# Optimization experiments

Measured on AMD Instinct MI355X. Metric: run time of the kernel, lower is better.

## Reference

```python
import jax, jax.numpy as jnp
import numpy as np

N_ROOMS = 128
N = 2 + N_ROOMS          # 2 external wall nodes + room nodes
T = 131072               # number of evaluation times
DT = 30.0                # seconds between evaluations
Q_LIM = 500.0
K_SCALE = 1e-5           # physical scaling of sigmoid(params) -> conductances [1/s]
DAY = 86400.0
TOUT_N = 1100            # hourly outside-temperature table covering the horizon


def setup_inputs() -> dict:
    key = jax.random.key(0)
    k1, k2, k3, k4 = jax.random.split(key, 4)
    t_eval = jnp.arange(T, dtype=jnp.float32) * DT
    params = jax.random.uniform(k1, (N * N,), dtype=jnp.float32)      # torch.rand init
    heating = jax.random.normal(k2, (N_ROOMS, 3), dtype=jnp.float32)  # torch.randn init
    B = jnp.zeros((N, 1 + N_ROOMS), dtype=jnp.float32)
    B = B.at[:, 0].set(jax.random.uniform(k3, (N,), dtype=jnp.float32) * 1e-5)  # Tout coupling
    B = B.at[2:, 1:].set(jnp.eye(N_ROOMS, dtype=jnp.float32) * 1e-6)           # heat input per room
    tout_t = jnp.arange(TOUT_N, dtype=jnp.float32) * 3600.0
    tout_v = 10.0 + 5.0 * jax.random.normal(k4, (TOUT_N,), dtype=jnp.float32)
    return {"t_eval": t_eval, "params": params, "heating": heating, "B": B,
            "tout_t": tout_t, "tout_v": tout_v}


def _forward(t_eval, params, heating, B, tout_t, tout_v):
    # transform + physical scaling of parameters -> RC conductance matrix A
    theta = jax.nn.sigmoid(params) * K_SCALE
    K = theta.reshape(N, N)
    d = jnp.diag(K)
    Koff = K - jnp.diag(d)
    A = Koff - jnp.diag(Koff.sum(axis=1) + d)   # Metzler, nonpositive row sums -> stable

    # transform + heat scaling -> continuous heating profile Qrms_continuous
    Q_avg = jax.nn.sigmoid(heating[:, 0]) * Q_LIM
    phase = heating[:, 1]
    sharp = heating[:, 2]

    t0 = t_eval[0]
    te = t_eval - t0
    two_pi = 2.0 * jnp.pi

    def Tout(t):  # Tout_continuous (linear interp, like scipy interp1d)
        return jnp.interp(t + t0, tout_t, tout_v)

    def Qf(t):    # smooth periodic heating schedule per room
        return Q_avg * jax.nn.sigmoid(sharp * jnp.sin(two_pi * (t + t0) / DAY + phase))

    def f(t, x):  # dx/dt = A @ x + B @ u
        u = jnp.concatenate([Tout(t)[None], Qf(t)])[:, None]   # [1+R, 1]
        return A @ x + B @ u

    iv = (Tout(te[0]) + 4.0) * jnp.ones((N, 1), dtype=jnp.float32)

    def step(x, tt):  # one RK4 step between consecutive evaluation times
        t, dt = tt
        half = dt * 0.5
        k1 = f(t, x)
        k2 = f(t + half, x + half * k1)
        k3 = f(t + half, x + half * k2)
        k4 = f(t + dt, x + dt * k3)
        xn = x + (dt / 6.0) * (k1 + 2.0 * k2 + 2.0 * k3 + k4)
        return xn, xn

    ts = te[:-1]
    dts = te[1:] - te[:-1]
    _, xs = jax.lax.scan(step, iv, (ts, dts))
    sol = jnp.concatenate([iv[None], xs], axis=0)   # [T, N, 1]
    return sol[:, 2:]                               # room temperatures only


def reference(t_eval, params, heating, B, tout_t, tout_v):
    return _forward(t_eval, params, heating, B, tout_t, tout_v)
```

## Files before the change

kernel.cpp:

```cpp
#include <hip/hip_runtime.h>
#include <math.h>

#define NPAD 132
#define TSTEPS 131071
#define LCH 128
#define NCH 1024
#define PERIOD 2880
#define OMEGA 7.2722052166430399e-05f

#define OFF_A    0
#define OFF_A2   17160
#define OFF_A3   34320
#define OFF_M    51480
#define OFF_C1   68640
#define OFF_C2   85800
#define OFF_P1   102960
#define OFF_P2   120120
#define OFF_M2   137280
#define OFF_M4   154440
#define OFF_M64  171600
#define OFF_M128 188760
#define OFF_M2K  205920
#define OFF_C1T  223080
#define OFF_C2T  239464
#define OFF_C1B  255848
#define OFF_C2B  255978
#define OFF_C3B  256108
#define OFF_AMP  256238
#define OFF_CPH  256366
#define OFF_SPH  256494
#define OFF_SH   256622
#define OFF_W    256750
#define OFF_G    257920
#define OFF_S64  391040
#define OFF_XB   524160
#define OFF_XB2  657280
#define OFF_SA   923520
#define OFF_GP   931710
#define OFF_GP2  1306110
#define OFF_GP4  1680510
#define OFF_TT   2054910

typedef float f4 __attribute__((ext_vector_type(4)));

#define MLOAD(Q, S) asm volatile("global_load_dwordx4 %0, %1, off offset:" S \
                                 : "=v"(mr[Q]) : "v"(base))
__device__ __forceinline__ void load_mrow(const float* base, f4* mr) {
    MLOAD(0, "0");    MLOAD(1, "16");   MLOAD(2, "32");   MLOAD(3, "48");
    MLOAD(4, "64");   MLOAD(5, "80");   MLOAD(6, "96");   MLOAD(7, "112");
    MLOAD(8, "128");  MLOAD(9, "144");  MLOAD(10, "160"); MLOAD(11, "176");
    MLOAD(12, "192"); MLOAD(13, "208"); MLOAD(14, "224"); MLOAD(15, "240");
    MLOAD(16, "256"); MLOAD(17, "272"); MLOAD(18, "288"); MLOAD(19, "304");
    MLOAD(20, "320"); MLOAD(21, "336"); MLOAD(22, "352"); MLOAD(23, "368");
    MLOAD(24, "384"); MLOAD(25, "400"); MLOAD(26, "416"); MLOAD(27, "432");
    MLOAD(28, "448"); MLOAD(29, "464"); MLOAD(30, "480"); MLOAD(31, "496");
    MLOAD(32, "512");
    asm volatile("s_waitcnt vmcnt(0)" ::: "memory");
    __builtin_amdgcn_sched_barrier(0);
}

__device__ __forceinline__ float sigm(float x) { return 1.0f / (1.0f + expf(-x)); }

__device__ __forceinline__ float interp_tout(float t, const float* __restrict__ tv) {
    float u = t * (1.0f / 3600.0f);
    int idx = (int)u;
    if (idx > 1098) idx = 1098;
    float fr = u - (float)idx;
    float v0 = tv[idx];
    return v0 + fr * (tv[idx + 1] - v0);
}

__global__ __launch_bounds__(256) void build_A_kernel(
    const float* __restrict__ params, const float* __restrict__ heating,
    const float* __restrict__ Bm, const float* __restrict__ tout_v,
    float* __restrict__ ws, float* __restrict__ out) {
    const int tid = threadIdx.x;
    float* A = ws + OFF_A;

    for (int idx = tid; idx < 130 * 130; idx += 256) {
        int r = idx / 130, c = idx - r * 130;
        A[r * NPAD + c] = sigm(params[idx]) * 1e-5f;
    }
    for (int r = tid; r < 130; r += 256) { A[r * NPAD + 130] = 0.f; A[r * NPAD + 131] = 0.f; }
    __syncthreads();
    for (int r = tid; r < 130; r += 256) {
        float s = 0.0f;
        for (int k = 0; k < 130; ++k) s += A[r * NPAD + k];
        A[r * NPAD + r] = -s;
    }
    for (int i = tid; i < 128; i += 256) {
        float bd = Bm[(2 + i) * 129 + (1 + i)];
        ws[OFF_AMP + i] = sigm(heating[i * 3]) * 500.0f * bd;
        float ph = heating[i * 3 + 1];
        ws[OFF_CPH + i] = cosf(ph);
        ws[OFF_SPH + i] = sinf(ph);
        ws[OFF_SH + i]  = heating[i * 3 + 2];
    }
    float iv = tout_v[0] + 4.0f;
    for (int i = tid; i < 128; i += 256) out[i] = iv;
    for (int r = tid; r < 130; r += 256) ws[OFF_XB + r] = iv;
}

__global__ __launch_bounds__(192) void mm_kernel(float* __restrict__ ws,
                                                 int offD, int offX, int offY) {
    const float* X = ws + offX;
    const float* Y = ws + offY;
    float* dst = ws + offD;
    __shared__ float xrow[130];
    const int r = blockIdx.x;
    const int c = threadIdx.x;
    if (c < 130) xrow[c] = X[r * NPAD + c];
    __syncthreads();
    if (c < 130) {
        float acc = 0.0f;
#pragma unroll 10
        for (int k = 0; k < 130; ++k)
            acc = fmaf(xrow[k], Y[k * NPAD + c], acc);
        dst[r * NPAD + c] = acc;
    }
    if (c >= 130 && c < 132) dst[r * NPAD + c] = 0.0f;
}

__global__ __launch_bounds__(192) void mm34_kernel(float* __restrict__ ws) {
    const int b = blockIdx.x;
    const bool hi = (b >= 130);
    const int r = hi ? b - 130 : b;
    const float* X = ws + (hi ? OFF_A2 : OFF_A);
    const float* Y = ws + OFF_A2;
    float* dst = ws + (hi ? OFF_P2 : OFF_A3);
    __shared__ float xrow[130];
    const int c = threadIdx.x;
    if (c < 130) xrow[c] = X[r * NPAD + c];
    __syncthreads();
    if (c < 130) {
        float acc = 0.0f;
#pragma unroll 10
        for (int k = 0; k < 130; ++k)
            acc = fmaf(xrow[k], Y[k * NPAD + c], acc);
        dst[r * NPAD + c] = acc;
    }
    if (c >= 130 && c < 132) dst[r * NPAD + c] = 0.0f;
}

__global__ __launch_bounds__(256) void combine_kernel(float* __restrict__ ws) {
    int idx = blockIdx.x * 256 + threadIdx.x;
    if (idx >= 130 * 130) return;
    int r = idx / 130, c = idx - r * 130;
    int o = r * NPAD + c;
    const float* A  = ws + OFF_A;
    const float* A2 = ws + OFF_A2;
    const float* A3 = ws + OFF_A3;
    const float* A4 = ws + OFF_P2;
    float eye = (r == c) ? 1.0f : 0.0f;
    float a = A[o], a2 = A2[o], a3 = A3[o], a4 = A4[o];
    float c1v = 5.0f * eye + 150.0f * a + 2250.0f * a2 + 33750.0f * a3;
    float c2v = 20.0f * eye + 300.0f * a + 2250.0f * a2;
    ws[OFF_M  + o] = eye + 30.0f * a + 450.0f * a2 + 4500.0f * a3 + 33750.0f * a4;
    ws[OFF_C1 + o] = c1v;
    ws[OFF_C2 + o] = c2v;
    if (r >= 2 && c >= 2) {
        ws[OFF_C1T + (c - 2) * 128 + (r - 2)] = c1v;
        ws[OFF_C2T + (c - 2) * 128 + (r - 2)] = c2v;
    }
    if (c == 0) {
        ws[OFF_M + r * NPAD + 130] = 0.f; ws[OFF_M + r * NPAD + 131] = 0.f;
        ws[OFF_C1 + r * NPAD + 130] = 0.f; ws[OFF_C1 + r * NPAD + 131] = 0.f;
        ws[OFF_C2 + r * NPAD + 130] = 0.f; ws[OFF_C2 + r * NPAD + 131] = 0.f;
    }
}

__global__ __launch_bounds__(192) void vecs2_kernel(const float* __restrict__ Bm,
                                                    float* __restrict__ ws) {
    const int r = threadIdx.x;
    const float* C1 = ws + OFF_C1;
    const float* C2 = ws + OFF_C2;
    const float* Mm = ws + OFF_M;
    __shared__ __align__(16) float va[132], vb[132], vd[132];
    __shared__ __align__(16) float na[132], nb[132], nd[132];
    __shared__ float a1s[130], a2s[130], c1bs[130];

    if (r < 132) { va[r] = 0.f; vb[r] = 0.f; vd[r] = 0.f; na[r] = 0.f; nb[r] = 0.f; nd[r] = 0.f; }
    __syncthreads();
    if (r < 130) {
        float s1 = 0.0f, s2 = 0.0f;
        for (int k = 0; k < 130; ++k) {
            float b0 = Bm[k * 129];
            s1 = fmaf(C1[r * NPAD + k], b0, s1);
            s2 = fmaf(C2[r * NPAD + k], b0, s2);
        }
        float c3 = 5.0f * Bm[r * 129];
        ws[OFF_C1B + r] = s1; ws[OFF_C2B + r] = s2; ws[OFF_C3B + r] = c3;
        ws[OFF_W + 7 * 130 + r] = s2;
        ws[OFF_W + 8 * 130 + r] = c3;
        va[r] = s1; vb[r] = s2; vd[r] = c3; c1bs[r] = s1;
    }
    __syncthreads();

    for (int st = 1; st <= 3; ++st) {
        if (r < 130) {
            const f4* mp = reinterpret_cast<const f4*>(&Mm[r * NPAD]);
            const f4* pa = reinterpret_cast<const f4*>(va);
            const f4* pb = reinterpret_cast<const f4*>(vb);
            const f4* pd = reinterpret_cast<const f4*>(vd);
            float aa = 0.f, ab = 0.f, ad = 0.f;
#pragma unroll
            for (int q = 0; q < 33; ++q) {
                f4 m = mp[q];
                f4 xa = pa[q], xb = pb[q], xd = pd[q];
                aa = fmaf(m.x, xa.x, fmaf(m.y, xa.y, fmaf(m.z, xa.z, fmaf(m.w, xa.w, aa))));
                ab = fmaf(m.x, xb.x, fmaf(m.y, xb.y, fmaf(m.z, xb.z, fmaf(m.w, xb.w, ab))));
                ad = fmaf(m.x, xd.x, fmaf(m.y, xd.y, fmaf(m.z, xd.z, fmaf(m.w, xd.w, ad))));
            }
            na[r] = aa; nb[r] = ab; nd[r] = ad;
        }
        __syncthreads();
        if (r < 130) {
            if (st == 1) { ws[OFF_W + 5 * 130 + r] = nb[r]; ws[OFF_W + 6 * 130 + r] = nd[r] + c1bs[r]; a1s[r] = na[r]; }
            if (st == 2) { ws[OFF_W + 3 * 130 + r] = nb[r]; ws[OFF_W + 4 * 130 + r] = nd[r] + a1s[r]; a2s[r] = na[r]; }
            if (st == 3) { ws[OFF_W + 0 * 130 + r] = na[r]; ws[OFF_W + 1 * 130 + r] = nb[r]; ws[OFF_W + 2 * 130 + r] = nd[r] + a2s[r]; }
            va[r] = na[r]; vb[r] = nb[r]; vd[r] = nd[r];
        }
        __syncthreads();
    }
}

__global__ __launch_bounds__(256) void gper_kernel(float* __restrict__ ws) {
    const int tid = threadIdx.x;
    const int n0 = blockIdx.x * 32;
    const float* C1T = ws + OFF_C1T;
    const float* C2T = ws + OFF_C2T;
    const float* C1 = ws + OFF_C1;
    const float* C2 = ws + OFF_C2;
    const float* amp = ws + OFF_AMP;
    const float* cph = ws + OFF_CPH;
    const float* sph = ws + OFF_SPH;
    const float* sh  = ws + OFF_SH;
    float* P = ws + OFF_GP;

    __shared__ __align__(16) float qgT[128][36];
    __shared__ __align__(16) float qmT[128][36];
    __shared__ float sth[65], cth[65];

    for (int j = tid; j < 65; j += 256) {
        float t = (j < 33) ? (float)(n0 + j) * 30.0f
                           : (float)(n0 + j - 33) * 30.0f + 15.0f;
        float a = t * OMEGA;
        sth[j] = sinf(a);
        cth[j] = cosf(a);
    }
    __syncthreads();

    for (int p = tid; p < 65 * 128; p += 256) {
        int j = p >> 7, i = p & 127;
        float s = sth[j] * cph[i] + cth[j] * sph[i];
        float v = amp[i] / (1.0f + __expf(-sh[i] * s));
        if (j < 33) qgT[i][j] = v; else qmT[i][j - 33] = v;
    }
    __syncthreads();

    const int rr = tid & 127;
    const int half = tid >> 7;
    const int r = rr + 2;
    float acc1[16], acc2[16];
#pragma unroll
    for (int w = 0; w < 16; ++w) { acc1[w] = 0.0f; acc2[w] = 0.0f; }

    for (int k = 0; k < 128; ++k) {
        float c1 = C1T[(k << 7) + rr];
        float c2 = C2T[(k << 7) + rr];
        const float4* q1p = reinterpret_cast<const float4*>(&qgT[k][half * 16]);
        const float4* q2p = reinterpret_cast<const float4*>(&qmT[k][half * 16]);
#pragma unroll
        for (int w = 0; w < 4; ++w) {
            float4 a = q1p[w];
            float4 b = q2p[w];
            acc1[4 * w + 0] = fmaf(c1, a.x, acc1[4 * w + 0]);
            acc1[4 * w + 1] = fmaf(c1, a.y, acc1[4 * w + 1]);
            acc1[4 * w + 2] = fmaf(c1, a.z, acc1[4 * w + 2]);
            acc1[4 * w + 3] = fmaf(c1, a.w, acc1[4 * w + 3]);
            acc2[4 * w + 0] = fmaf(c2, b.x, acc2[4 * w + 0]);
            acc2[4 * w + 1] = fmaf(c2, b.y, acc2[4 * w + 1]);
            acc2[4 * w + 2] = fmaf(c2, b.z, acc2[4 * w + 2]);
            acc2[4 * w + 3] = fmaf(c2, b.w, acc2[4 * w + 3]);
        }
    }
#pragma unroll
    for (int w = 0; w < 16; ++w) {
        int n = half * 16 + w;
        P[(n0 + n) * 130 + r] = acc1[w] + acc2[w] + 5.0f * qgT[rr][n + 1];
    }

    if (tid < 64) {
        int r2 = tid >> 5;
        int n = tid & 31;
        float acc = 0.0f;
        for (int k = 0; k < 128; ++k) {
            acc = fmaf(C1[r2 * NPAD + 2 + k], qgT[k][n], acc);
            acc = fmaf(C2[r2 * NPAD + 2 + k], qmT[k][n], acc);
        }
        P[(n0 + n) * 130 + r2] = acc;
    }
}

__global__ __launch_bounds__(192) void pdouble_kernel(float* __restrict__ ws,
                                                      int offD, int offS, int offMat, int shift) {
    const int m0 = blockIdx.x * 16;
    const int tid = threadIdx.x;
    const float* S = ws + offS;
    const float* Mat = ws + offMat;
    float* D = ws + offD;
    __shared__ __align__(16) float xs2[16][132];
    for (int p = tid; p < 16 * 132; p += 192) {
        int i = p / 132, rr = p - i * 132;
        xs2[i][rr] = (rr < 130) ? S[(m0 + i) * 130 + rr] : 0.0f;
    }
    __syncthreads();
    const int r = tid;
    if (r < 130) {
        float acc[16];
#pragma unroll
        for (int i = 0; i < 16; ++i) acc[i] = 0.0f;
        const f4* mp = reinterpret_cast<const f4*>(&Mat[r * NPAD]);
        for (int q = 0; q < 33; ++q) {
            f4 m = mp[q];
#pragma unroll
            for (int i = 0; i < 16; ++i) {
                f4 x = reinterpret_cast<const f4*>(xs2[i])[q];
                acc[i] = fmaf(m.x, x.x, fmaf(m.y, x.y, fmaf(m.z, x.z, fmaf(m.w, x.w, acc[i]))));
            }
        }
#pragma unroll
        for (int i = 0; i < 16; ++i) {
            int ms = m0 + i + shift; if (ms >= PERIOD) ms -= PERIOD;
            D[(m0 + i) * 130 + r] = acc[i] + S[ms * 130 + r];
        }
    }
}

__global__ __launch_bounds__(256) void ttab_kernel(const float* __restrict__ tout_v,
                                                   float* __restrict__ ws) {
    int n = blockIdx.x * 256 + threadIdx.x;
    if (n < 131080) {
        float t = (float)n * 30.0f;
        float2* TT = reinterpret_cast<float2*>(ws + OFF_TT);
        TT[n] = make_float2(interp_tout(t, tout_v), interp_tout(t + 15.0f, tout_v));
    }
}

__global__ __launch_bounds__(192, 2) void chunk_accum_kernel(float* __restrict__ ws) {
    const int c = blockIdx.x;
    const int r = threadIdx.x;
    const float* M4 = ws + OFF_M4;
    const float* P4 = ws + OFF_GP4;
    const float2* TT = reinterpret_cast<const float2*>(ws + OFF_TT);

    __shared__ __align__(16) float xs[2][132];
    f4 mr[33];
    float w0 = 0.f, w1 = 0.f, w2 = 0.f, w3 = 0.f, w4 = 0.f, w5 = 0.f, w6 = 0.f, w7 = 0.f, w8 = 0.f;
    if (r < 130) {
        load_mrow(&M4[r * NPAD], mr);
        w0 = ws[OFF_W + 0 * 130 + r]; w1 = ws[OFF_W + 1 * 130 + r]; w2 = ws[OFF_W + 2 * 130 + r];
        w3 = ws[OFF_W + 3 * 130 + r]; w4 = ws[OFF_W + 4 * 130 + r]; w5 = ws[OFF_W + 5 * 130 + r];
        w6 = ws[OFF_W + 6 * 130 + r]; w7 = ws[OFF_W + 7 * 130 + r]; w8 = ws[OFF_W + 8 * 130 + r];
    }
    if (r < 132) { xs[0][r] = 0.0f; xs[1][r] = 0.0f; }
    __syncthreads();

    const int base = c * LCH;
    int mu = base % PERIOD;
    float pv = (r < 130) ? P4[mu * 130 + r] : 0.0f;
    int cur = 0;
    for (int u = 0; u < 32; ++u) {
        if (r < 130) {
            const int n = base + 4 * u;
            float2 t0 = TT[n], t1 = TT[n + 1], t2 = TT[n + 2], t3 = TT[n + 3];
            float tg4 = TT[n + 4].x;
            float gcur = pv
                + t0.x * w0 + t0.y * w1 + t1.x * w2 + t1.y * w3
                + t2.x * w4 + t2.y * w5 + t3.x * w6 + t3.y * w7 + tg4 * w8;
            mu = (mu + 4 >= PERIOD) ? mu + 4 - PERIOD : mu + 4;
            if (u + 1 < 32) pv = P4[mu * 130 + r];
            const f4* xp = reinterpret_cast<const f4*>(xs[cur]);
            float a0 = 0.f, a1 = 0.f, a2 = 0.f, a3 = 0.f;
#pragma unroll
            for (int q = 0; q < 33; ++q) {
                f4 xv = xp[q];
                a0 = fmaf(mr[q].x, xv.x, a0);
                a1 = fmaf(mr[q].y, xv.y, a1);
                a2 = fmaf(mr[q].z, xv.z, a2);
                a3 = fmaf(mr[q].w, xv.w, a3);
            }
            float val = (a0 + a1) + (a2 + a3) + gcur;
            xs[cur ^ 1][r] = val;
            if (u == 15) ws[OFF_S64 + c * 130 + r] = val;
        }
        __syncthreads();
        cur ^= 1;
    }
    if (r < 130) ws[OFF_G + c * 130 + r] = xs[cur][r];
}

__global__ __launch_bounds__(192, 2) void superaccum_kernel(float* __restrict__ ws) {
    const int s = blockIdx.x;
    const int r = threadIdx.x;
    const float* MP = ws + OFF_M128;
    const float* G = ws + OFF_G;

    __shared__ __align__(16) float xs[2][132];
    f4 mr[33];
    if (r < 130) load_mrow(&MP[r * NPAD], mr);
    if (r < 132) { xs[0][r] = 0.0f; xs[1][r] = 0.0f; }
    __syncthreads();

    int cur = 0;
    for (int i = 0; i < 16; ++i) {
        if (r < 130) {
            const f4* xp = reinterpret_cast<const f4*>(xs[cur]);
            float a0 = 0.f, a1 = 0.f, a2 = 0.f, a3 = 0.f;
#pragma unroll
            for (int q = 0; q < 33; ++q) {
                f4 xv = xp[q];
                a0 = fmaf(mr[q].x, xv.x, a0);
                a1 = fmaf(mr[q].y, xv.y, a1);
                a2 = fmaf(mr[q].z, xv.z, a2);
                a3 = fmaf(mr[q].w, xv.w, a3);
            }
            xs[cur ^ 1][r] = (a0 + a1) + (a2 + a3) + G[(16 * s + i) * 130 + r];
        }
        __syncthreads();
        cur ^= 1;
    }
    if (r < 130) ws[OFF_SA + s * 130 + r] = xs[cur][r];
}

__global__ __launch_bounds__(192, 2) void superbound_kernel(float* __restrict__ ws) {
    const int r = threadIdx.x;
    const float* M2K = ws + OFF_M2K;
    const float* SA = ws + OFF_SA;
    float* xb = ws + OFF_XB;

    __shared__ __align__(16) float xs[2][132];
    f4 mr[33];
    if (r < 130) load_mrow(&M2K[r * NPAD], mr);
    if (r < 132) { xs[0][r] = (r < 130) ? xb[r] : 0.0f; xs[1][r] = 0.0f; }
    __syncthreads();

    int cur = 0;
    for (int s = 0; s < 63; ++s) {
        if (r < 130) {
            const f4* xp = reinterpret_cast<const f4*>(xs[cur]);
            float a0 = 0.f, a1 = 0.f, a2 = 0.f, a3 = 0.f;
#pragma unroll
            for (int q = 0; q < 33; ++q) {
                f4 xv = xp[q];
                a0 = fmaf(mr[q].x, xv.x, a0);
                a1 = fmaf(mr[q].y, xv.y, a1);
                a2 = fmaf(mr[q].z, xv.z, a2);
                a3 = fmaf(mr[q].w, xv.w, a3);
            }
            float val = (a0 + a1) + (a2 + a3) + SA[s * 130 + r];
            xs[cur ^ 1][r] = val;
            xb[(16 * s + 16) * 130 + r] = val;
        }
        __syncthreads();
        cur ^= 1;
    }
}

__global__ __launch_bounds__(192, 2) void chunkbound_kernel(float* __restrict__ ws) {
    const int s = blockIdx.x;
    const int r = threadIdx.x;
    const float* MP = ws + OFF_M128;
    const float* G = ws + OFF_G;
    float* xb = ws + OFF_XB;

    __shared__ __align__(16) float xs[2][132];
    f4 mr[33];
    if (r < 130) load_mrow(&MP[r * NPAD], mr);
    if (r < 132) { xs[0][r] = (r < 130) ? xb[(16 * s) * 130 + r] : 0.0f; xs[1][r] = 0.0f; }
    __syncthreads();

    int cur = 0;
    for (int i = 0; i < 15; ++i) {
        if (r < 130) {
            const f4* xp = reinterpret_cast<const f4*>(xs[cur]);
            float a0 = 0.f, a1 = 0.f, a2 = 0.f, a3 = 0.f;
#pragma unroll
            for (int q = 0; q < 33; ++q) {
                f4 xv = xp[q];
                a0 = fmaf(mr[q].x, xv.x, a0);
                a1 = fmaf(mr[q].y, xv.y, a1);
                a2 = fmaf(mr[q].z, xv.z, a2);
                a3 = fmaf(mr[q].w, xv.w, a3);
            }
            float val = (a0 + a1) + (a2 + a3) + G[(16 * s + i) * 130 + r];
            xs[cur ^ 1][r] = val;
            xb[(16 * s + i + 1) * 130 + r] = val;
        }
        __syncthreads();
        cur ^= 1;
    }
}

__global__ __launch_bounds__(192, 2) void subbound_kernel(float* __restrict__ ws) {
    const int c = blockIdx.x;
    const int r = threadIdx.x;
    const float* M64 = ws + OFF_M64;
    const float* xb = ws + OFF_XB;
    float* xb2 = ws + OFF_XB2;

    __shared__ __align__(16) float xs[132];
    if (r < 132) xs[r] = (r < 130) ? xb[c * 130 + r] : 0.0f;
    __syncthreads();
    if (r < 130) {
        const f4* xp = reinterpret_cast<const f4*>(xs);
        const f4* mp = reinterpret_cast<const f4*>(&M64[r * NPAD]);
        float a0 = 0.f, a1 = 0.f, a2 = 0.f, a3 = 0.f;
#pragma unroll
        for (int q = 0; q < 33; ++q) {
            f4 m = mp[q];
            f4 xv = xp[q];
            a0 = fmaf(m.x, xv.x, a0);
            a1 = fmaf(m.y, xv.y, a1);
            a2 = fmaf(m.z, xv.z, a2);
            a3 = fmaf(m.w, xv.w, a3);
        }
        xb2[(2 * c) * 130 + r] = xs[r];
        xb2[(2 * c + 1) * 130 + r] = (a0 + a1) + (a2 + a3) + ws[OFF_S64 + c * 130 + r];
    }
}

__global__ __launch_bounds__(192, 2) void chunk_emit_kernel(float* __restrict__ ws,
                                                            float* __restrict__ out) {
    const int ec = blockIdx.x;
    const int r = threadIdx.x;
    const float* Mm = ws + OFF_M;
    const float* P = ws + OFF_GP;
    const float2* TT = reinterpret_cast<const float2*>(ws + OFF_TT);
    const float* xb2 = ws + OFF_XB2;

    __shared__ __align__(16) float xs[2][132];
    f4 mr[33];
    float c1br = 0.f, c2br = 0.f, c3br = 0.f;
    if (r < 130) {
        load_mrow(&Mm[r * NPAD], mr);
        c1br = ws[OFF_C1B + r]; c2br = ws[OFF_C2B + r]; c3br = ws[OFF_C3B + r];
    }
    if (r < 132) { xs[0][r] = (r < 130) ? xb2[ec * 130 + r] : 0.0f; xs[1][r] = 0.0f; }
    __syncthreads();

    const int base = ec * 64;
    const int len = min(64, TSTEPS - base);
    int m = base % PERIOD;
    float pv = (r < 130) ? P[m * 130 + r] : 0.0f;
    float2 tc = TT[base], tn = TT[base + 1];
    int cur = 0;
    for (int j = 0; j < len; ++j) {
        if (r < 130) {
            float gcur = pv + tc.x * c1br + tc.y * c2br + tn.x * c3br;
            m = (m + 1 == PERIOD) ? 0 : m + 1;
            if (j + 1 < len) { pv = P[m * 130 + r]; tc = tn; tn = TT[base + j + 2]; }
            const f4* xp = reinterpret_cast<const f4*>(xs[cur]);
            float a0 = 0.f, a1 = 0.f, a2 = 0.f, a3 = 0.f;
#pragma unroll
            for (int q = 0; q < 33; ++q) {
                f4 xv = xp[q];
                a0 = fmaf(mr[q].x, xv.x, a0);
                a1 = fmaf(mr[q].y, xv.y, a1);
                a2 = fmaf(mr[q].z, xv.z, a2);
                a3 = fmaf(mr[q].w, xv.w, a3);
            }
            float val = (a0 + a1) + (a2 + a3) + gcur;
            xs[cur ^ 1][r] = val;
            if (r >= 2) out[(base + j + 1) * 128 + (r - 2)] = val;
        }
        __syncthreads();
        cur ^= 1;
    }
}

extern "C" void kernel_launch(void* const* d_in, const int* in_sizes, int n_in,
                              void* d_out, int out_size, void* d_ws, size_t ws_size,
                              hipStream_t stream) {
    const float* params  = (const float*)d_in[1];
    const float* heating = (const float*)d_in[2];
    const float* Bm      = (const float*)d_in[3];
    const float* tout_v  = (const float*)d_in[5];
    float* out = (float*)d_out;
    float* ws = (float*)d_ws;

    build_A_kernel<<<1, 256, 0, stream>>>(params, heating, Bm, tout_v, ws, out);

    mm_kernel<<<130, 192, 0, stream>>>(ws, OFF_A2, OFF_A, OFF_A);
    mm34_kernel<<<260, 192, 0, stream>>>(ws);
    combine_kernel<<<67, 256, 0, stream>>>(ws);
    vecs2_kernel<<<1, 192, 0, stream>>>(Bm, ws);
    gper_kernel<<<90, 256, 0, stream>>>(ws);
    ttab_kernel<<<513, 256, 0, stream>>>(tout_v, ws);

    mm_kernel<<<130, 192, 0, stream>>>(ws, OFF_M2,   OFF_M,    OFF_M);
    mm_kernel<<<130, 192, 0, stream>>>(ws, OFF_M4,   OFF_M2,   OFF_M2);
    mm_kernel<<<130, 192, 0, stream>>>(ws, OFF_P1,   OFF_M4,   OFF_M4);
    mm_kernel<<<130, 192, 0, stream>>>(ws, OFF_P2,   OFF_P1,   OFF_P1);
    mm_kernel<<<130, 192, 0, stream>>>(ws, OFF_P1,   OFF_P2,   OFF_P2);
    mm_kernel<<<130, 192, 0, stream>>>(ws, OFF_M64,  OFF_P1,   OFF_P1);
    mm_kernel<<<130, 192, 0, stream>>>(ws, OFF_M128, OFF_M64,  OFF_M64);
    mm_kernel<<<130, 192, 0, stream>>>(ws, OFF_P1,   OFF_M128, OFF_M128);
    mm_kernel<<<130, 192, 0, stream>>>(ws, OFF_P2,   OFF_P1,   OFF_P1);
    mm_kernel<<<130, 192, 0, stream>>>(ws, OFF_P1,   OFF_P2,   OFF_P2);
    mm_kernel<<<130, 192, 0, stream>>>(ws, OFF_M2K,  OFF_P1,   OFF_P1);

    pdouble_kernel<<<180, 192, 0, stream>>>(ws, OFF_GP2, OFF_GP,  OFF_M,  1);
    pdouble_kernel<<<180, 192, 0, stream>>>(ws, OFF_GP4, OFF_GP2, OFF_M2, 2);

    chunk_accum_kernel<<<NCH, 192, 0, stream>>>(ws);
    superaccum_kernel<<<63, 192, 0, stream>>>(ws);
    superbound_kernel<<<1, 192, 0, stream>>>(ws);
    chunkbound_kernel<<<64, 192, 0, stream>>>(ws);
    subbound_kernel<<<NCH, 192, 0, stream>>>(ws);
    chunk_emit_kernel<<<2 * NCH, 192, 0, stream>>>(ws, out);
}
```

Measured before the change: 505.2 us.

## Split each matrix-row dot product across four lanes with shuffle reduction

The sequential matvec-recurrence kernels now use four threads per state row, each holding a 36-column slice of the matrix row in registers and reducing partial sums with xor shuffles. This cuts per-thread FMA chain length and register use from 33 to 9 vector registers, shortening the latency of each serial step. The cost is 576-thread blocks with more barrier participants, padded shared arrays, and shuffle overhead per step; the subbound kernel's min-blocks hint is dropped.

```diff
diff --git a/kernel.cpp b/kernel.cpp
--- a/kernel.cpp
+++ b/kernel.cpp
@@ -43,20 +43,31 @@
 
 typedef float f4 __attribute__((ext_vector_type(4)));
 
-#define MLOAD(Q, S) asm volatile("global_load_dwordx4 %0, %1, off offset:" S \
-                                 : "=v"(mr[Q]) : "v"(base))
-__device__ __forceinline__ void load_mrow(const float* base, f4* mr) {
-    MLOAD(0, "0");    MLOAD(1, "16");   MLOAD(2, "32");   MLOAD(3, "48");
-    MLOAD(4, "64");   MLOAD(5, "80");   MLOAD(6, "96");   MLOAD(7, "112");
-    MLOAD(8, "128");  MLOAD(9, "144");  MLOAD(10, "160"); MLOAD(11, "176");
-    MLOAD(12, "192"); MLOAD(13, "208"); MLOAD(14, "224"); MLOAD(15, "240");
-    MLOAD(16, "256"); MLOAD(17, "272"); MLOAD(18, "288"); MLOAD(19, "304");
-    MLOAD(20, "320"); MLOAD(21, "336"); MLOAD(22, "352"); MLOAD(23, "368");
-    MLOAD(24, "384"); MLOAD(25, "400"); MLOAD(26, "416"); MLOAD(27, "432");
-    MLOAD(28, "448"); MLOAD(29, "464"); MLOAD(30, "480"); MLOAD(31, "496");
-    MLOAD(32, "512");
+#define MLOAD9(Q, S) asm volatile("global_load_dwordx4 %0, %1, off offset:" S \
+                                  : "=v"(mr[Q]) : "v"(mb))
+__device__ __forceinline__ void load_mslice(const float* mb, f4* mr) {
+    MLOAD9(0, "0");   MLOAD9(1, "16");  MLOAD9(2, "32");
+    MLOAD9(3, "48");  MLOAD9(4, "64");  MLOAD9(5, "80");
+    MLOAD9(6, "96");  MLOAD9(7, "112"); MLOAD9(8, "128");
     asm volatile("s_waitcnt vmcnt(0)" ::: "memory");
     __builtin_amdgcn_sched_barrier(0);
+}
+
+__device__ __forceinline__ float qdot(const f4* mr, const float* xsrow, int h) {
+    const f4* xp = reinterpret_cast<const f4*>(xsrow) + h * 9;
+    float a0 = 0.f, a1 = 0.f, a2 = 0.f, a3 = 0.f;
+#pragma unroll
+    for (int q = 0; q < 9; ++q) {
+        f4 xv = xp[q];
+        a0 = fmaf(mr[q].x, xv.x, a0);
+        a1 = fmaf(mr[q].y, xv.y, a1);
+        a2 = fmaf(mr[q].z, xv.z, a2);
+        a3 = fmaf(mr[q].w, xv.w, a3);
+    }
+    float s = (a0 + a1) + (a2 + a3);
+    s += __shfl_xor(s, 1);
+    s += __shfl_xor(s, 2);
+    return s;
 }
 
 __device__ __forceinline__ float sigm(float x) { return 1.0f / (1.0f + expf(-x)); }
@@ -347,31 +358,35 @@
     }
 }
 
-__global__ __launch_bounds__(192, 2) void chunk_accum_kernel(float* __restrict__ ws) {
+__global__ __launch_bounds__(576) void chunk_accum_kernel(float* __restrict__ ws) {
     const int c = blockIdx.x;
-    const int r = threadIdx.x;
-    const float* M4 = ws + OFF_M4;
+    const int t = threadIdx.x;
+    const int r = t >> 2;
+    const int h = t & 3;
+    const bool act = (r < 130);
     const float* P4 = ws + OFF_GP4;
     const float2* TT = reinterpret_cast<const float2*>(ws + OFF_TT);
 
-    __shared__ __align__(16) float xs[2][132];
-    f4 mr[33];
+    __shared__ __align__(16) float xs[2][144];
+    f4 mr[9];
+    const float* mb = &ws[OFF_M4 + r * NPAD + h * 36];
+    load_mslice(mb, mr);
     float w0 = 0.f, w1 = 0.f, w2 = 0.f, w3 = 0.f, w4 = 0.f, w5 = 0.f, w6 = 0.f, w7 = 0.f, w8 = 0.f;
-    if (r < 130) {
-        load_mrow(&M4[r * NPAD], mr);
+    if (act && h == 0) {
         w0 = ws[OFF_W + 0 * 130 + r]; w1 = ws[OFF_W + 1 * 130 + r]; w2 = ws[OFF_W + 2 * 130 + r];
         w3 = ws[OFF_W + 3 * 130 + r]; w4 = ws[OFF_W + 4 * 130 + r]; w5 = ws[OFF_W + 5 * 130 + r];
         w6 = ws[OFF_W + 6 * 130 + r]; w7 = ws[OFF_W + 7 * 130 + r]; w8 = ws[OFF_W + 8 * 130 + r];
     }
-    if (r < 132) { xs[0][r] = 0.0f; xs[1][r] = 0.0f; }
+    if (t < 144) { xs[0][t] = 0.0f; xs[1][t] = 0.0f; }
     __syncthreads();
 
     const int base = c * LCH;
     int mu = base % PERIOD;
-    float pv = (r < 130) ? P4[mu * 130 + r] : 0.0f;
+    float pv = (act && h == 0) ? P4[mu * 130 + r] : 0.0f;
     int cur = 0;
     for (int u = 0; u < 32; ++u) {
-        if (r < 130) {
+        float s = qdot(mr, xs[cur], h);
+        if (act && h == 0) {
             const int n = base + 4 * u;
             float2 t0 = TT[n], t1 = TT[n + 1], t2 = TT[n + 2], t3 = TT[n + 3];
             float tg4 = TT[n + 4].x;
@@ -380,85 +395,62 @@
                 + t2.x * w4 + t2.y * w5 + t3.x * w6 + t3.y * w7 + tg4 * w8;
             mu = (mu + 4 >= PERIOD) ? mu + 4 - PERIOD : mu + 4;
             if (u + 1 < 32) pv = P4[mu * 130 + r];
-            const f4* xp = reinterpret_cast<const f4*>(xs[cur]);
-            float a0 = 0.f, a1 = 0.f, a2 = 0.f, a3 = 0.f;
-#pragma unroll
-            for (int q = 0; q < 33; ++q) {
-                f4 xv = xp[q];
-                a0 = fmaf(mr[q].x, xv.x, a0);
-                a1 = fmaf(mr[q].y, xv.y, a1);
-                a2 = fmaf(mr[q].z, xv.z, a2);
-                a3 = fmaf(mr[q].w, xv.w, a3);
-            }
-            float val = (a0 + a1) + (a2 + a3) + gcur;
+            float val = s + gcur;
             xs[cur ^ 1][r] = val;
             if (u == 15) ws[OFF_S64 + c * 130 + r] = val;
         }
         __syncthreads();
         cur ^= 1;
     }
-    if (r < 130) ws[OFF_G + c * 130 + r] = xs[cur][r];
-}
-
-__global__ __launch_bounds__(192, 2) void superaccum_kernel(float* __restrict__ ws) {
+    if (act && h == 0) ws[OFF_G + c * 130 + r] = xs[cur][r];
+}
+
+__global__ __launch_bounds__(576) void superaccum_kernel(float* __restrict__ ws) {
     const int s = blockIdx.x;
-    const int r = threadIdx.x;
-    const float* MP = ws + OFF_M128;
+    const int t = threadIdx.x;
+    const int r = t >> 2;
+    const int h = t & 3;
+    const bool act = (r < 130);
     const float* G = ws + OFF_G;
 
-    __shared__ __align__(16) float xs[2][132];
-    f4 mr[33];
-    if (r < 130) load_mrow(&MP[r * NPAD], mr);
-    if (r < 132) { xs[0][r] = 0.0f; xs[1][r] = 0.0f; }
+    __shared__ __align__(16) float xs[2][144];
+    f4 mr[9];
+    const float* mb = &ws[OFF_M128 + r * NPAD + h * 36];
+    load_mslice(mb, mr);
+    if (t < 144) { xs[0][t] = 0.0f; xs[1][t] = 0.0f; }
     __syncthreads();
 
     int cur = 0;
     for (int i = 0; i < 16; ++i) {
-        if (r < 130) {
-            const f4* xp = reinterpret_cast<const f4*>(xs[cur]);
-            float a0 = 0.f, a1 = 0.f, a2 = 0.f, a3 = 0.f;
-#pragma unroll
-            for (int q = 0; q < 33; ++q) {
-                f4 xv = xp[q];
-                a0 = fmaf(mr[q].x, xv.x, a0);
-                a1 = fmaf(mr[q].y, xv.y, a1);
-                a2 = fmaf(mr[q].z, xv.z, a2);
-                a3 = fmaf(mr[q].w, xv.w, a3);
-            }
-            xs[cur ^ 1][r] = (a0 + a1) + (a2 + a3) + G[(16 * s + i) * 130 + r];
-        }
+        float sum = qdot(mr, xs[cur], h);
+        if (act && h == 0)
+            xs[cur ^ 1][r] = sum + G[(16 * s + i) * 130 + r];
         __syncthreads();
         cur ^= 1;
     }
-    if (r < 130) ws[OFF_SA + s * 130 + r] = xs[cur][r];
-}
-
-__global__ __launch_bounds__(192, 2) void superbound_kernel(float* __restrict__ ws) {
-    const int r = threadIdx.x;
-    const float* M2K = ws + OFF_M2K;
+    if (act && h == 0) ws[OFF_SA + s * 130 + r] = xs[cur][r];
+}
+
+__global__ __launch_bounds__(576) void superbound_kernel(float* __restrict__ ws) {
+    const int t = threadIdx.x;
+    const int r = t >> 2;
+    const int h = t & 3;
+    const bool act = (r < 130);
     const float* SA = ws + OFF_SA;
     float* xb = ws + OFF_XB;
 
-    __shared__ __align__(16) float xs[2][132];
-    f4 mr[33];
-    if (r < 130) load_mrow(&M2K[r * NPAD], mr);
-    if (r < 132) { xs[0][r] = (r < 130) ? xb[r] : 0.0f; xs[1][r] = 0.0f; }
+    __shared__ __align__(16) float xs[2][144];
+    f4 mr[9];
+    const float* mb = &ws[OFF_M2K + r * NPAD + h * 36];
+    load_mslice(mb, mr);
+    if (t < 144) { xs[0][t] = (t < 130) ? xb[t] : 0.0f; xs[1][t] = 0.0f; }
     __syncthreads();
 
     int cur = 0;
     for (int s = 0; s < 63; ++s) {
-        if (r < 130) {
-            const f4* xp = reinterpret_cast<const f4*>(xs[cur]);
-            float a0 = 0.f, a1 = 0.f, a2 = 0.f, a3 = 0.f;
-#pragma unroll
-            for (int q = 0; q < 33; ++q) {
-                f4 xv = xp[q];
-                a0 = fmaf(mr[q].x, xv.x, a0);
-                a1 = fmaf(mr[q].y, xv.y, a1);
-                a2 = fmaf(mr[q].z, xv.z, a2);
-                a3 = fmaf(mr[q].w, xv.w, a3);
-            }
-            float val = (a0 + a1) + (a2 + a3) + SA[s * 130 + r];
+        float sum = qdot(mr, xs[cur], h);
+        if (act && h == 0) {
+            float val = sum + SA[s * 130 + r];
             xs[cur ^ 1][r] = val;
             xb[(16 * s + 16) * 130 + r] = val;
         }
@@ -467,33 +459,27 @@
     }
 }
 
-__global__ __launch_bounds__(192, 2) void chunkbound_kernel(float* __restrict__ ws) {
+__global__ __launch_bounds__(576) void chunkbound_kernel(float* __restrict__ ws) {
     const int s = blockIdx.x;
-    const int r = threadIdx.x;
-    const float* MP = ws + OFF_M128;
+    const int t = threadIdx.x;
+    const int r = t >> 2;
+    const int h = t & 3;
+    const bool act = (r < 130);
     const float* G = ws + OFF_G;
     float* xb = ws + OFF_XB;
 
-    __shared__ __align__(16) float xs[2][132];
-    f4 mr[33];
-    if (r < 130) load_mrow(&MP[r * NPAD], mr);
-    if (r < 132) { xs[0][r] = (r < 130) ? xb[(16 * s) * 130 + r] : 0.0f; xs[1][r] = 0.0f; }
+    __shared__ __align__(16) float xs[2][144];
+    f4 mr[9];
+    const float* mb = &ws[OFF_M128 + r * NPAD + h * 36];
+    load_mslice(mb, mr);
+    if (t < 144) { xs[0][t] = (t < 130) ? xb[(16 * s) * 130 + t] : 0.0f; xs[1][t] = 0.0f; }
     __syncthreads();
 
     int cur = 0;
     for (int i = 0; i < 15; ++i) {
-        if (r < 130) {
-            const f4* xp = reinterpret_cast<const f4*>(xs[cur]);
-            float a0 = 0.f, a1 = 0.f, a2 = 0.f, a3 = 0.f;
-#pragma unroll
-            for (int q = 0; q < 33; ++q) {
-                f4 xv = xp[q];
-                a0 = fmaf(mr[q].x, xv.x, a0);
-                a1 = fmaf(mr[q].y, xv.y, a1);
-                a2 = fmaf(mr[q].z, xv.z, a2);
-                a3 = fmaf(mr[q].w, xv.w, a3);
-            }
-            float val = (a0 + a1) + (a2 + a3) + G[(16 * s + i) * 130 + r];
+        float sum = qdot(mr, xs[cur], h);
+        if (act && h == 0) {
+            float val = sum + G[(16 * s + i) * 130 + r];
             xs[cur ^ 1][r] = val;
             xb[(16 * s + i + 1) * 130 + r] = val;
         }
@@ -502,7 +488,7 @@
     }
 }
 
-__global__ __launch_bounds__(192, 2) void subbound_kernel(float* __restrict__ ws) {
+__global__ __launch_bounds__(192) void subbound_kernel(float* __restrict__ ws) {
     const int c = blockIdx.x;
     const int r = threadIdx.x;
     const float* M64 = ws + OFF_M64;
@@ -530,47 +516,42 @@
     }
 }
 
-__global__ __launch_bounds__(192, 2) void chunk_emit_kernel(float* __restrict__ ws,
-                                                            float* __restrict__ out) {
+__global__ __launch_bounds__(576) void chunk_emit_kernel(float* __restrict__ ws,
+                                                         float* __restrict__ out) {
     const int ec = blockIdx.x;
-    const int r = threadIdx.x;
-    const float* Mm = ws + OFF_M;
+    const int t = threadIdx.x;
+    const int r = t >> 2;
+    const int h = t & 3;
+    const bool act = (r < 130);
     const float* P = ws + OFF_GP;
     const float2* TT = reinterpret_cast<const float2*>(ws + OFF_TT);
     const float* xb2 = ws + OFF_XB2;
 
-    __shared__ __align__(16) float xs[2][132];
-    f4 mr[33];
+    __shared__ __align__(16) float xs[2][144];
+    f4 mr[9];
+    const float* mb = &ws[OFF_M + r * NPAD + h * 36];
+    load_mslice(mb, mr);
     float c1br = 0.f, c2br = 0.f, c3br = 0.f;
-    if (r < 130) {
-        load_mrow(&Mm[r * NPAD], mr);
+    if (act && h == 0) {
         c1br = ws[OFF_C1B + r]; c2br = ws[OFF_C2B + r]; c3br = ws[OFF_C3B + r];
     }
-    if (r < 132) { xs[0][r] = (r < 130) ? xb2[ec * 130 + r] : 0.0f; xs[1][r] = 0.0f; }
+    if (t < 144) { xs[0][t] = (t < 130) ? xb2[ec * 130 + t] : 0.0f; xs[1][t] = 0.0f; }
     __syncthreads();
 
     const int base = ec * 64;
     const int len = min(64, TSTEPS - base);
     int m = base % PERIOD;
-    float pv = (r < 130) ? P[m * 130 + r] : 0.0f;
-    float2 tc = TT[base], tn = TT[base + 1];
+    float pv = 0.f;
+    float2 tc = make_float2(0.f, 0.f), tn = make_float2(0.f, 0.f);
+    if (act && h == 0) { pv = P[m * 130 + r]; tc = TT[base]; tn = TT[base + 1]; }
     int cur = 0;
     for (int j = 0; j < len; ++j) {
-        if (r < 130) {
+        float s = qdot(mr, xs[cur], h);
+        if (act && h == 0) {
             float gcur = pv + tc.x * c1br + tc.y * c2br + tn.x * c3br;
             m = (m + 1 == PERIOD) ? 0 : m + 1;
             if (j + 1 < len) { pv = P[m * 130 + r]; tc = tn; tn = TT[base + j + 2]; }
-            const f4* xp = reinterpret_cast<const f4*>(xs[cur]);
-            float a0 = 0.f, a1 = 0.f, a2 = 0.f, a3 = 0.f;
-#pragma unroll
-            for (int q = 0; q < 33; ++q) {
-                f4 xv = xp[q];
-                a0 = fmaf(mr[q].x, xv.x, a0);
-                a1 = fmaf(mr[q].y, xv.y, a1);
-                a2 = fmaf(mr[q].z, xv.z, a2);
-                a3 = fmaf(mr[q].w, xv.w, a3);
-            }
-            float val = (a0 + a1) + (a2 + a3) + gcur;
+            float val = s + gcur;
             xs[cur ^ 1][r] = val;
             if (r >= 2) out[(base + j + 1) * 128 + (r - 2)] = val;
         }
@@ -613,10 +594,10 @@
     pdouble_kernel<<<180, 192, 0, stream>>>(ws, OFF_GP2, OFF_GP,  OFF_M,  1);
     pdouble_kernel<<<180, 192, 0, stream>>>(ws, OFF_GP4, OFF_GP2, OFF_M2, 2);
 
-    chunk_accum_kernel<<<NCH, 192, 0, stream>>>(ws);
-    superaccum_kernel<<<63, 192, 0, stream>>>(ws);
-    superbound_kernel<<<1, 192, 0, stream>>>(ws);
-    chunkbound_kernel<<<64, 192, 0, stream>>>(ws);
+    chunk_accum_kernel<<<NCH, 576, 0, stream>>>(ws);
+    superaccum_kernel<<<63, 576, 0, stream>>>(ws);
+    superbound_kernel<<<1, 576, 0, stream>>>(ws);
+    chunkbound_kernel<<<64, 576, 0, stream>>>(ws);
     subbound_kernel<<<NCH, 192, 0, stream>>>(ws);
-    chunk_emit_kernel<<<2 * NCH, 192, 0, stream>>>(ws, out);
-}
+    chunk_emit_kernel<<<2 * NCH, 576, 0, stream>>>(ws, out);
+}
```

Result: slower. 575.4 us (+13.9%).
